# Kernel optimization log

Measured on AMD Instinct MI355X. Metric: run time of the kernel, lower is better.

The kernel has to match this reference:

```python
import jax, jax.numpy as jnp
import numpy as np

N_NODES = 10000

def rgcn_layer(x, edge_index, basis, comp, root, bias):
    # x: [N, Fin]; edge_index: [R, 2, E] int; basis: [B, Fin, Fout]; comp: [R, B]
    R, _, E = edge_index.shape
    N = x.shape[0]
    src = edge_index[:, 0]  # [R, E]
    dst = edge_index[:, 1]  # [R, E]
    # basis-decomposed per-relation weights: W_r = sum_b comp[r,b] * basis[b]
    W = jnp.einsum('rb,bio->rio', comp, basis)          # [R, Fin, Fout]
    x_src = x[src]                                       # [R, E, Fin] gather
    msg = jnp.einsum('rei,rio->reo', x_src, W)           # [R, E, Fout]
    # per-relation mean aggregation onto destination nodes
    seg = (jnp.arange(R, dtype=dst.dtype)[:, None] * N + dst).reshape(-1)  # [R*E]
    agg = jax.ops.segment_sum(msg.reshape(R * E, -1), seg, num_segments=R * N)
    deg = jax.ops.segment_sum(jnp.ones((R * E,), x.dtype), seg, num_segments=R * N)
    agg = agg / jnp.maximum(deg, 1.0)[:, None]
    agg = agg.reshape(R, N, -1).sum(0)                   # sum over relations
    return agg + x @ root + bias


def setup_inputs() -> dict:
    key = jax.random.key(0)
    ks = jax.random.split(key, 10)
    s = 0.05  # scale params for numerical sanity
    return {
        'x_drug': jax.random.normal(ks[0], (N_NODES, 2048), jnp.float32),
        'drug_w': jax.random.normal(ks[1], (2048, 128), jnp.float32) * s,
        'edge_index': jax.random.randint(ks[2], (100, 2, 5000), 0, N_NODES, jnp.int32),
        'basis1': jax.random.normal(ks[3], (8, 128, 64), jnp.float32) * s,
        'comp1': jax.random.normal(ks[4], (100, 8), jnp.float32) * s,
        'root1': jax.random.normal(ks[5], (128, 64), jnp.float32) * s,
        'bias1': jnp.zeros((64,), jnp.float32),
        'basis2': jax.random.normal(ks[6], (8, 64, 20), jnp.float32) * s,
        'comp2': jax.random.normal(ks[7], (100, 8), jnp.float32) * s,
        'root2': jax.random.normal(ks[8], (64, 20), jnp.float32) * s,
        'bias2': jnp.zeros((20,), jnp.float32),
    }


def reference(x_drug, drug_w, edge_index, basis1, comp1, root1, bias1,
              basis2, comp2, root2, bias2):
    x = x_drug @ drug_w                                   # dense projection [N, 128]
    h = rgcn_layer(x, edge_index, basis1, comp1, root1, bias1)   # [N, 64]
    h = jax.nn.relu(h)
    out = rgcn_layer(h, edge_index, basis2, comp2, root2, bias2)  # [N, 20]
    return out
```

## Files before the change

kernel.cpp:

```cpp
#include <hip/hip_runtime.h>

#define NN 10000
#define RR 100
#define EE 5000
#define D0 2048
#define D1 128
#define D2 64
#define D3 20
#define NE (RR*EE)
#define MAXD 128

using short8  = __attribute__((ext_vector_type(8))) short;
using float4e = __attribute__((ext_vector_type(4))) float;

typedef const __attribute__((address_space(1))) void g_void;
typedef __attribute__((address_space(3))) void l_void;

__device__ __forceinline__ unsigned short f2bf(float f) {
  unsigned int u = __float_as_uint(f);
  unsigned int r = u + 0x7fffu + ((u >> 16) & 1u);
  return (unsigned short)(r >> 16);
}
__device__ __forceinline__ float bf2f(unsigned short u) {
  return __uint_as_float(((unsigned int)u) << 16);
}
__device__ __forceinline__ unsigned int pk2(float lo, float hi) {
  return ((unsigned int)f2bf(hi) << 16) | (unsigned int)f2bf(lo);
}

#define CURB 10
#define WTBLK 1024
#define W1BLK 288
#define W2BLK 72
__global__ __launch_bounds__(256) void prep_kernel(
    const float* __restrict__ W, const float* __restrict__ root1,
    const float* __restrict__ basis1, const float* __restrict__ root2,
    const float* __restrict__ basis2, int4* __restrict__ cur4,
    unsigned short* __restrict__ Btw, unsigned short* __restrict__ Wc1T,
    unsigned short* __restrict__ Wc2T) {
  const int b = blockIdx.x, tid = threadIdx.x;
  if (b < CURB) {
    int i = b * 256 + tid;
    if (i < 2504) cur4[i] = make_int4(0, 0, 0, 0);
  } else if (b < CURB + WTBLK) {
    int idx = (b - CURB) * 256 + tid;
    int n = idx >> 11, k = idx & 2047;
    Btw[idx] = f2bf(W[(size_t)k * 128 + n]);
  } else if (b < CURB + WTBLK + W1BLK) {
    int idx = (b - CURB - WTBLK) * 256 + tid;
    int o = idx / 1152, j = idx - o * 1152;
    float v = (j < 128) ? root1[j * 64 + o] : basis1[(j - 128) * 64 + o];
    Wc1T[idx] = f2bf(v);
  } else {
    int idx = (b - CURB - WTBLK - W1BLK) * 256 + tid;
    int c = idx / 576, j = idx - c * 576;
    float v = 0.f;
    if (c < 20) v = (j < 64) ? root2[j * 20 + c] : basis2[(j - 64) * 20 + c];
    Wc2T[idx] = f2bf(v);
  }
}

__global__ void scatter_kernel(const int* __restrict__ ei,
                               int* __restrict__ cur, int* __restrict__ rec) {
  int gid = blockIdx.x * 256 + threadIdx.x;
  if (gid >= NE) return;
  int r = gid / EE, e = gid - r * EE;
  int s = ei[r * 2 * EE + e];
  int d = ei[r * 2 * EE + EE + e];
  int p = atomicAdd(&cur[d], 1);
  if (p < MAXD) rec[d * MAXD + p] = (r << 14) | s;
}

__global__ __launch_bounds__(256, 3) void gemm0_mfma(
    const float* __restrict__ A, const unsigned short* __restrict__ Btw,
    unsigned short* __restrict__ xb) {
  __shared__ __align__(16) unsigned short Asb[2][16 * 64];
  __shared__ __align__(16) unsigned short Bsb[3][128 * 64];
  const int tid = threadIdx.x;
  const int m0 = blockIdx.x * 16;
  const int wv = tid >> 6, lane = tid & 63;
  const int lrow = lane & 15, quad = lane >> 4;

  const int ar = tid >> 4, ag = tid & 15;
  const float* Ap = &A[(size_t)(m0 + ar) * D0 + ag * 4];
  const int aw = (ar * 128 + ((ag * 8) ^ ((ar & 7) << 4))) >> 1;

  const int rowB = wv * 32 + (lane >> 3);
  const int gch  = (lane & 7) ^ (lane >> 3);
  const unsigned short* BgBase = &Btw[(size_t)rowB * D0 + gch * 8];
  const int ldsB = wv * 2048;

  float4 a0, a1;

#define G0_LOADB(buf, c)                                                     \
  { _Pragma("unroll")                                                        \
    for (int i = 0; i < 4; i++) {                                            \
      __builtin_amdgcn_global_load_lds(                                      \
          (g_void*)(BgBase + (size_t)i * 8 * D0 + (c) * 64),                 \
          (l_void*)&Bsb[buf][ldsB + i * 512], 16, 0, 0);                     \
    } }

#define G0_LOADA(reg, c)  { reg = *(const float4*)(Ap + (c) * 64); }

#define G0_PACKA(reg, buf)                                              \
  { uint2 p0;                                                           \
    p0.x = pk2(reg.x, reg.y); p0.y = pk2(reg.z, reg.w);                 \
    *(uint2*)&Asb[buf][aw] = p0; }

#define G0_COMPUTE(abuf, bbuf)                                          \
  { const int aswz = (lrow & 7) << 4;                                   \
    _Pragma("unroll")                                                   \
    for (int kk = 0; kk < 2; kk++) {                                    \
      short8 af = *(const short8*)&Asb[abuf][(lrow * 128 + ((quad * 16 + kk * 64) ^ aswz)) >> 1]; \
      _Pragma("unroll")                                                 \
      for (int nt = 0; nt < 2; nt++) {                                  \
        const int brow = wv * 32 + nt * 16 + lrow;                      \
        short8 bfr = *(const short8*)&Bsb[bbuf][(brow * 128 + ((quad * 16 + kk * 64) ^ ((brow & 7) << 4))) >> 1]; \
        acc[nt] = __builtin_amdgcn_mfma_f32_16x16x32_bf16(af, bfr, acc[nt], 0, 0, 0); \
      }                                                                 \
    } }

  float4e acc[2];
#pragma unroll
  for (int i = 0; i < 2; i++) { acc[i][0]=0.f; acc[i][1]=0.f; acc[i][2]=0.f; acc[i][3]=0.f; }

  G0_LOADA(a0, 0);
  G0_LOADB(0, 0);
  G0_LOADB(1, 1);
  G0_PACKA(a0, 0);
  G0_LOADA(a1, 1);
  asm volatile("s_waitcnt vmcnt(5) lgkmcnt(0)\ns_barrier" ::: "memory");

#pragma unroll
  for (int c = 0; c < 32; c++) {
    if (c <= 29) {
      G0_LOADB((c + 2) % 3, c + 2);
      if ((c & 1) == 0) { G0_LOADA(a0, c + 2); }
      else              { G0_LOADA(a1, c + 2); }
      __builtin_amdgcn_sched_barrier(0);
    }
    G0_COMPUTE(c & 1, c % 3);
    if (c <= 30) {
      if (((c + 1) & 1) == 0) { G0_PACKA(a0, 0); }
      else                    { G0_PACKA(a1, 1); }
      asm volatile("s_waitcnt vmcnt(5) lgkmcnt(0)\ns_barrier" ::: "memory");
    }
  }

#pragma unroll
  for (int nt = 0; nt < 2; nt++) {
    const int col = wv * 32 + nt * 16 + lrow;
#pragma unroll
    for (int r = 0; r < 4; r++) {
      const int row = m0 + quad * 4 + r;
      xb[(size_t)row * D1 + col] = f2bf(acc[nt][r]);
    }
  }
}

__global__ __launch_bounds__(256) void agg1e_kernel(
    const unsigned short* __restrict__ xb, const int* __restrict__ cur,
    const int* __restrict__ rec, const float* __restrict__ comp,
    unsigned short* __restrict__ A1b) {
  __shared__ float s_comp[RR * 8];
  __shared__ float s_rcp[4][RR];
  const int tid = threadIdx.x;
  for (int i = tid; i < RR * 8; i += 256) s_comp[i] = comp[i];
  const int wv = tid >> 6, lane = tid & 63;
  const int n = blockIdx.x * 4 + wv;
  int* hist = (int*)&s_rcp[wv][0];
  for (int i = lane; i < RR; i += 64) hist[i] = 0;
  __syncthreads();
  int cnt = cur[n]; if (cnt > MAXD) cnt = MAXD;
  if (lane < cnt)      atomicAdd(&hist[rec[n * MAXD + lane] >> 14], 1);
  if (lane + 64 < cnt) atomicAdd(&hist[rec[n * MAXD + lane + 64] >> 14], 1);
  __syncthreads();
  for (int i = lane; i < RR; i += 64) {
    int h = hist[i];
    s_rcp[wv][i] = 1.0f / (float)h;
  }
  __syncthreads();

  float acc[8][2];
#pragma unroll
  for (int b = 0; b < 8; b++) { acc[b][0] = 0.f; acc[b][1] = 0.f; }
  const int beg = n * MAXD, end = beg + cnt;
  int idx = beg;
  for (; idx + 3 < end; idx += 4) {
    int rc[4]; float sc[4]; unsigned int xv[4];
#pragma unroll
    for (int u = 0; u < 4; u++) rc[u] = rec[idx + u];
#pragma unroll
    for (int u = 0; u < 4; u++) sc[u] = s_rcp[wv][rc[u] >> 14];
#pragma unroll
    for (int u = 0; u < 4; u++)
      xv[u] = *(const unsigned int*)&xb[(size_t)(rc[u] & 16383) * D1 + lane * 2];
#pragma unroll
    for (int u = 0; u < 4; u++) {
      const float* cb = &s_comp[(rc[u] >> 14) * 8];
      float x0 = __uint_as_float((xv[u] & 0xffffu) << 16);
      float x1 = __uint_as_float(xv[u] & 0xffff0000u);
#pragma unroll
      for (int b = 0; b < 8; b++) {
        float w = sc[u] * cb[b];
        acc[b][0] += w * x0;
        acc[b][1] += w * x1;
      }
    }
  }
  for (; idx < end; idx++) {
    int rc = rec[idx];
    float sc = s_rcp[wv][rc >> 14];
    unsigned int xv = *(const unsigned int*)&xb[(size_t)(rc & 16383) * D1 + lane * 2];
    const float* cb = &s_comp[(rc >> 14) * 8];
    float x0 = __uint_as_float((xv & 0xffffu) << 16);
    float x1 = __uint_as_float(xv & 0xffff0000u);
#pragma unroll
    for (int b = 0; b < 8; b++) {
      float w = sc * cb[b];
      acc[b][0] += w * x0;
      acc[b][1] += w * x1;
    }
  }
#pragma unroll
  for (int b = 0; b < 8; b++) {
    ushort2 o; o.x = f2bf(acc[b][0]); o.y = f2bf(acc[b][1]);
    *(ushort2*)&A1b[(size_t)n * 1024 + b * 128 + lane * 2] = o;
  }
}

__global__ __launch_bounds__(256) void agg2e_kernel(
    const unsigned short* __restrict__ hb, const int* __restrict__ cur,
    const int* __restrict__ rec, const float* __restrict__ comp,
    unsigned short* __restrict__ A2b) {
  __shared__ float s_comp[RR * 8];
  __shared__ float s_rcp[4][RR];
  const int tid = threadIdx.x;
  for (int i = tid; i < RR * 8; i += 256) s_comp[i] = comp[i];
  const int wv = tid >> 6, lane = tid & 63;
  const int n = blockIdx.x * 4 + wv;
  int* hist = (int*)&s_rcp[wv][0];
  for (int i = lane; i < RR; i += 64) hist[i] = 0;
  __syncthreads();
  int cnt = cur[n]; if (cnt > MAXD) cnt = MAXD;
  if (lane < cnt)      atomicAdd(&hist[rec[n * MAXD + lane] >> 14], 1);
  if (lane + 64 < cnt) atomicAdd(&hist[rec[n * MAXD + lane + 64] >> 14], 1);
  __syncthreads();
  for (int i = lane; i < RR; i += 64) {
    int h = hist[i];
    s_rcp[wv][i] = 1.0f / (float)h;
  }
  __syncthreads();

  float acc[8];
#pragma unroll
  for (int b = 0; b < 8; b++) acc[b] = 0.f;
  const int beg = n * MAXD, end = beg + cnt;
  int idx = beg;
  for (; idx + 3 < end; idx += 4) {
    int rc[4]; float sc[4]; float hv[4];
#pragma unroll
    for (int u = 0; u < 4; u++) rc[u] = rec[idx + u];
#pragma unroll
    for (int u = 0; u < 4; u++) sc[u] = s_rcp[wv][rc[u] >> 14];
#pragma unroll
    for (int u = 0; u < 4; u++)
      hv[u] = bf2f(hb[(size_t)(rc[u] & 16383) * D2 + lane]);
#pragma unroll
    for (int u = 0; u < 4; u++) {
      const float* cb = &s_comp[(rc[u] >> 14) * 8];
#pragma unroll
      for (int b = 0; b < 8; b++) acc[b] += sc[u] * cb[b] * hv[u];
    }
  }
  for (; idx < end; idx++) {
    int rc = rec[idx];
    float sc = s_rcp[wv][rc >> 14];
    float hv = bf2f(hb[(size_t)(rc & 16383) * D2 + lane]);
    const float* cb = &s_comp[(rc >> 14) * 8];
#pragma unroll
    for (int b = 0; b < 8; b++) acc[b] += sc * cb[b] * hv;
  }
#pragma unroll
  for (int b = 0; b < 8; b++)
    A2b[(size_t)n * 512 + b * 64 + lane] = f2bf(acc[b]);
}

__global__ __launch_bounds__(256) void hlayer_mfma(
    const unsigned short* __restrict__ xb, const unsigned short* __restrict__ A1b,
    const unsigned short* __restrict__ Wt, const float* __restrict__ bias1,
    unsigned short* __restrict__ hb) {
  __shared__ __align__(16) unsigned short Asb[2][32 * 64];
  __shared__ __align__(16) unsigned short Bsb[2][64 * 64];
  const int tid = threadIdx.x;
  const int m0 = blockIdx.x * 32;
  const int wv = tid >> 6, lane = tid & 63;
  const int lrow = lane & 15, quad = lane >> 4;
  const int mt = wv >> 1, nb = wv & 1;

  const int ar = tid >> 3, ac = tid & 7;
  int gr = m0 + ar; if (gr >= NN) gr = NN - 1;
  const unsigned short* Ax = &xb[(size_t)gr * D1 + ac * 8];
  const unsigned short* Aa = &A1b[(size_t)gr * 1024 + ac * 8];
  const int asw = (ar & 7) << 4;
  const int aw = (ar * 128 + ((ac * 16) ^ asw)) >> 1;

  const int br = tid >> 2, bq = tid & 3;
  const unsigned short* Bp = &Wt[(size_t)br * 1152 + bq * 16];
  const int bsw = (br & 7) << 4;
  const int bw0 = (br * 128 + ((bq * 32) ^ bsw)) >> 1;
  const int bw1 = (br * 128 + ((bq * 32 + 16) ^ bsw)) >> 1;

  uint4 ra, rb0, rb1;

#define H_LOADG(c)                                                       \
  { int kb = (c) * 64;                                                   \
    ra  = (kb < 128) ? *(const uint4*)(Ax + kb)                          \
                     : *(const uint4*)(Aa + (kb - 128));                 \
    rb0 = *(const uint4*)(Bp + kb);                                      \
    rb1 = *(const uint4*)(Bp + kb + 8); }

#define H_STOREL(buf)                                                    \
  { *(uint4*)&Asb[buf][aw]  = ra;                                        \
    *(uint4*)&Bsb[buf][bw0] = rb0;                                       \
    *(uint4*)&Bsb[buf][bw1] = rb1; }

#define H_COMPUTE(buf)                                                   \
  { const int arow = mt * 16 + lrow;                                     \
    const int aswz = (arow & 7) << 4;                                    \
    _Pragma("unroll")                                                    \
    for (int kk = 0; kk < 2; kk++) {                                     \
      short8 af = *(const short8*)&Asb[buf][(arow * 128 + ((quad * 16 + kk * 64) ^ aswz)) >> 1]; \
      _Pragma("unroll")                                                  \
      for (int nt = 0; nt < 2; nt++) {                                   \
        const int brow = nb * 32 + nt * 16 + lrow;                       \
        short8 bfr = *(const short8*)&Bsb[buf][(brow * 128 + ((quad * 16 + kk * 64) ^ ((brow & 7) << 4))) >> 1]; \
        acc[nt] = __builtin_amdgcn_mfma_f32_16x16x32_bf16(af, bfr, acc[nt], 0, 0, 0); \
      }                                                                  \
    } }

  float4e acc[2];
#pragma unroll
  for (int i = 0; i < 2; i++) { acc[i][0]=0.f; acc[i][1]=0.f; acc[i][2]=0.f; acc[i][3]=0.f; }

  H_LOADG(0);
  H_STOREL(0);
  __syncthreads();

#pragma unroll
  for (int c = 0; c < 18; c++) {
    if (c < 17) {
      H_LOADG(c + 1);
      __builtin_amdgcn_sched_barrier(0);
    }
    H_COMPUTE(c & 1);
    if (c < 17) H_STOREL((c + 1) & 1);
    __syncthreads();
  }

#pragma unroll
  for (int nt = 0; nt < 2; nt++) {
    int col = nb * 32 + nt * 16 + lrow;
    float bv = bias1[col];
#pragma unroll
    for (int r = 0; r < 4; r++) {
      int row = m0 + mt * 16 + quad * 4 + r;
      if (row < NN)
        hb[(size_t)row * D2 + col] = f2bf(fmaxf(acc[nt][r] + bv, 0.f));
    }
  }
}

__global__ __launch_bounds__(256) void out_mfma(
    const unsigned short* __restrict__ hb, const unsigned short* __restrict__ A2b,
    const unsigned short* __restrict__ Wt, const float* __restrict__ bias2,
    float* __restrict__ out) {
  __shared__ __align__(16) unsigned short Asb[2][32 * 64];
  __shared__ __align__(16) unsigned short Bsb[2][32 * 64];
  const int tid = threadIdx.x;
  const int m0 = blockIdx.x * 32;
  const int wv = tid >> 6, lane = tid & 63;
  const int lrow = lane & 15, quad = lane >> 4;
  const int mt = wv >> 1, ntn = wv & 1;

  const int ar = tid >> 3, ac = tid & 7;
  int gr = m0 + ar; if (gr >= NN) gr = NN - 1;
  const unsigned short* Ah = &hb[(size_t)gr * D2 + ac * 8];
  const unsigned short* Aa = &A2b[(size_t)gr * 512 + ac * 8];
  const unsigned short* Bp = &Wt[(size_t)ar * 576 + ac * 8];
  const int asw = (ar & 7) << 4;
  const int aw = (ar * 128 + ((ac * 16) ^ asw)) >> 1;

  uint4 ra, rb;

#define O_LOADG(c)                                                       \
  { int kb = (c) * 64;                                                   \
    ra = (kb < 64) ? *(const uint4*)(Ah)                                 \
                   : *(const uint4*)(Aa + (kb - 64));                    \
    rb = *(const uint4*)(Bp + kb); }

#define O_STOREL(buf)                                                    \
  { *(uint4*)&Asb[buf][aw] = ra;                                         \
    *(uint4*)&Bsb[buf][aw] = rb; }

#define O_COMPUTE(buf)                                                   \
  { const int arow = mt * 16 + lrow;                                     \
    const int aswz = (arow & 7) << 4;                                    \
    const int brow = ntn * 16 + lrow;                                    \
    const int bswz = (brow & 7) << 4;                                    \
    _Pragma("unroll")                                                    \
    for (int kk = 0; kk < 2; kk++) {                                     \
      short8 af = *(const short8*)&Asb[buf][(arow * 128 + ((quad * 16 + kk * 64) ^ aswz)) >> 1]; \
      short8 bfr = *(const short8*)&Bsb[buf][(brow * 128 + ((quad * 16 + kk * 64) ^ bswz)) >> 1]; \
      acc = __builtin_amdgcn_mfma_f32_16x16x32_bf16(af, bfr, acc, 0, 0, 0); \
    } }

  float4e acc;
  acc[0]=0.f; acc[1]=0.f; acc[2]=0.f; acc[3]=0.f;

  O_LOADG(0);
  O_STOREL(0);
  __syncthreads();

#pragma unroll
  for (int c = 0; c < 9; c++) {
    if (c < 8) {
      O_LOADG(c + 1);
      __builtin_amdgcn_sched_barrier(0);
    }
    O_COMPUTE(c & 1);
    if (c < 8) O_STOREL((c + 1) & 1);
    __syncthreads();
  }

  int col = ntn * 16 + lrow;
  if (col < D3) {
    float bv = bias2[col];
#pragma unroll
    for (int r = 0; r < 4; r++) {
      int row = m0 + mt * 16 + quad * 4 + r;
      if (row < NN)
        out[(size_t)row * D3 + col] = acc[r] + bv;
    }
  }
}

extern "C" void kernel_launch(void* const* d_in, const int* in_sizes, int n_in,
                              void* d_out, int out_size, void* d_ws,
                              size_t ws_size, hipStream_t stream) {
  const float* x_drug = (const float*)d_in[0];
  const float* drug_w = (const float*)d_in[1];
  const int*   ei     = (const int*)d_in[2];
  const float* basis1 = (const float*)d_in[3];
  const float* comp1  = (const float*)d_in[4];
  const float* root1  = (const float*)d_in[5];
  const float* bias1  = (const float*)d_in[6];
  const float* basis2 = (const float*)d_in[7];
  const float* comp2  = (const float*)d_in[8];
  const float* root2  = (const float*)d_in[9];
  const float* bias2  = (const float*)d_in[10];
  float* out = (float*)d_out;

  float* ws = (float*)d_ws;
  int*   cur  = (int*)ws;
  int*   rec  = cur + 10016;
  unsigned short* xb   = (unsigned short*)(rec + NN * MAXD);
  unsigned short* hb   = (unsigned short*)((float*)xb + 640000);
  unsigned short* Btw  = (unsigned short*)((float*)hb + 320000);
  unsigned short* Wc1T = (unsigned short*)((float*)Btw + 131072);
  unsigned short* Wc2T = (unsigned short*)((float*)Wc1T + 36864);
  float* R1 = (float*)Wc2T + 9216;
  unsigned short* A1b = (unsigned short*)R1;
  unsigned short* A2b = (unsigned short*)R1;

  prep_kernel<<<CURB + WTBLK + W1BLK + W2BLK, 256, 0, stream>>>(
      drug_w, root1, basis1, root2, basis2, (int4*)cur, Btw, Wc1T, Wc2T);

  scatter_kernel<<<(NE + 255) / 256, 256, 0, stream>>>(ei, cur, rec);

  gemm0_mfma<<<NN / 16, 256, 0, stream>>>(x_drug, Btw, xb);

  agg1e_kernel<<<NN / 4, 256, 0, stream>>>(xb, cur, rec, comp1, A1b);
  hlayer_mfma<<<(NN + 31) / 32, 256, 0, stream>>>(xb, A1b, Wc1T, bias1, hb);

  agg2e_kernel<<<NN / 4, 256, 0, stream>>>(hb, cur, rec, comp2, A2b);
  out_mfma<<<(NN + 31) / 32, 256, 0, stream>>>(hb, A2b, Wc2T, bias2, out);
}
```

Baseline: 147.6 us.

## Retile dense projection GEMM into 64x32 tiles with half-K B staging

The first dense GEMM now gives each block 64 rows by 32 output columns, with each wave owning 16 private rows, instead of giving each block 16 rows by all 128 columns. The 32-column B slice is staged into LDS in two large halves, which removes the per-K-step block barriers, and A loads use a deeper three-register prefetch. This cuts how much of B each block reads. In exchange, each A row is now read by four blocks, so more fp32 A traffic goes through cache, and LDS use rises while the occupancy hint drops from three blocks to two.

After: 183.0 us. 1.24x slower.

```diff
diff --git a/kernel.cpp b/kernel.cpp
--- a/kernel.cpp
+++ b/kernel.cpp
@@ -71,89 +71,105 @@
   if (p < MAXD) rec[d * MAXD + p] = (r << 14) | s;
 }
 
-__global__ __launch_bounds__(256, 3) void gemm0_mfma(
+__global__ __launch_bounds__(256, 2) void gemm0_mfma(
     const float* __restrict__ A, const unsigned short* __restrict__ Btw,
     unsigned short* __restrict__ xb) {
-  __shared__ __align__(16) unsigned short Asb[2][16 * 64];
-  __shared__ __align__(16) unsigned short Bsb[3][128 * 64];
+  __shared__ __align__(16) unsigned short Bsb[32 * 1024];
+  __shared__ __align__(16) unsigned short Asb[4][2][16 * 64];
   const int tid = threadIdx.x;
-  const int m0 = blockIdx.x * 16;
   const int wv = tid >> 6, lane = tid & 63;
+  const int mtile = blockIdx.x >> 2, nt4 = blockIdx.x & 3;
+  const int m0 = mtile * 64;
+  const int n0 = nt4 * 32;
   const int lrow = lane & 15, quad = lane >> 4;
 
-  const int ar = tid >> 4, ag = tid & 15;
-  const float* Ap = &A[(size_t)(m0 + ar) * D0 + ag * 4];
-  const int aw = (ar * 128 + ((ag * 8) ^ ((ar & 7) << 4))) >> 1;
-
-  const int rowB = wv * 32 + (lane >> 3);
-  const int gch  = (lane & 7) ^ (lane >> 3);
-  const unsigned short* BgBase = &Btw[(size_t)rowB * D0 + gch * 8];
-  const int ldsB = wv * 2048;
-
-  float4 a0, a1;
-
-#define G0_LOADB(buf, c)                                                     \
-  { _Pragma("unroll")                                                        \
-    for (int i = 0; i < 4; i++) {                                            \
-      __builtin_amdgcn_global_load_lds(                                      \
-          (g_void*)(BgBase + (size_t)i * 8 * D0 + (c) * 64),                 \
-          (l_void*)&Bsb[buf][ldsB + i * 512], 16, 0, 0);                     \
+  const int ar = lane >> 2, aq = lane & 3;
+  int gra = m0 + wv * 16 + ar; if (gra >= NN) gra = NN - 1;
+  const float* Ap = &A[(size_t)gra * D0 + aq * 16];
+  const int asw = (ar & 7) << 4;
+  const int aw0 = (ar * 128 + ((aq * 32) ^ asw)) >> 1;
+  const int aw1 = (ar * 128 + ((aq * 32 + 16) ^ asw)) >> 1;
+
+#define G0_STAGEB(half)                                                     \
+  { _Pragma("unroll")                                                       \
+    for (int j = 0; j < 16; j++) {                                          \
+      const int it  = wv * 16 + j;                                          \
+      const int row = it >> 1;                                              \
+      const int kb  = (it & 1) * 512;                                       \
+      const unsigned short* src = &Btw[(size_t)(n0 + row) * D0 +            \
+          (half) * 1024 + kb + ((lane * 8) ^ ((row & 7) << 3))];            \
+      __builtin_amdgcn_global_load_lds((g_void*)src,                        \
+          (l_void*)&Bsb[it * 512 + lane * 8], 16, 0, 0);                    \
     } }
 
-#define G0_LOADA(reg, c)  { reg = *(const float4*)(Ap + (c) * 64); }
-
-#define G0_PACKA(reg, buf)                                              \
-  { uint2 p0;                                                           \
-    p0.x = pk2(reg.x, reg.y); p0.y = pk2(reg.z, reg.w);                 \
-    *(uint2*)&Asb[buf][aw] = p0; }
-
-#define G0_COMPUTE(abuf, bbuf)                                          \
-  { const int aswz = (lrow & 7) << 4;                                   \
-    _Pragma("unroll")                                                   \
-    for (int kk = 0; kk < 2; kk++) {                                    \
-      short8 af = *(const short8*)&Asb[abuf][(lrow * 128 + ((quad * 16 + kk * 64) ^ aswz)) >> 1]; \
-      _Pragma("unroll")                                                 \
-      for (int nt = 0; nt < 2; nt++) {                                  \
-        const int brow = wv * 32 + nt * 16 + lrow;                      \
-        short8 bfr = *(const short8*)&Bsb[bbuf][(brow * 128 + ((quad * 16 + kk * 64) ^ ((brow & 7) << 4))) >> 1]; \
-        acc[nt] = __builtin_amdgcn_mfma_f32_16x16x32_bf16(af, bfr, acc[nt], 0, 0, 0); \
-      }                                                                 \
+#define G0_LOADA(R, c)                                                      \
+  { _Pragma("unroll")                                                       \
+    for (int j = 0; j < 4; j++)                                             \
+      R[j] = *(const float4*)(Ap + (size_t)(c) * 64 + j * 4); }
+
+#define G0_PACKA(R, buf)                                                    \
+  { uint4 p, q;                                                             \
+    p.x = pk2(R[0].x, R[0].y); p.y = pk2(R[0].z, R[0].w);                   \
+    p.z = pk2(R[1].x, R[1].y); p.w = pk2(R[1].z, R[1].w);                   \
+    q.x = pk2(R[2].x, R[2].y); q.y = pk2(R[2].z, R[2].w);                   \
+    q.z = pk2(R[3].x, R[3].y); q.w = pk2(R[3].z, R[3].w);                   \
+    *(uint4*)&Asb[wv][buf][aw0] = p;                                        \
+    *(uint4*)&Asb[wv][buf][aw1] = q; }
+
+#define G0_COMPUTE(abuf, c)                                                 \
+  { const int aswz = (lrow & 7) << 4;                                       \
+    _Pragma("unroll")                                                       \
+    for (int kk = 0; kk < 2; kk++) {                                        \
+      short8 af = *(const short8*)&Asb[wv][abuf][(lrow * 128 + ((kk * 64 + quad * 16) ^ aswz)) >> 1]; \
+      _Pragma("unroll")                                                     \
+      for (int ntl = 0; ntl < 2; ntl++) {                                   \
+        const int brow = ntl * 16 + lrow;                                   \
+        short8 bfr = *(const short8*)&Bsb[brow * 1024 + ((((c & 15) * 128 + kk * 64 + quad * 16) ^ ((brow & 7) << 4)) >> 1)]; \
+        acc[ntl] = __builtin_amdgcn_mfma_f32_16x16x32_bf16(af, bfr, acc[ntl], 0, 0, 0); \
+      }                                                                     \
     } }
 
+  float4 Ra[4], Rb[4], Rc[4];
   float4e acc[2];
 #pragma unroll
   for (int i = 0; i < 2; i++) { acc[i][0]=0.f; acc[i][1]=0.f; acc[i][2]=0.f; acc[i][3]=0.f; }
 
-  G0_LOADA(a0, 0);
-  G0_LOADB(0, 0);
-  G0_LOADB(1, 1);
-  G0_PACKA(a0, 0);
-  G0_LOADA(a1, 1);
-  asm volatile("s_waitcnt vmcnt(5) lgkmcnt(0)\ns_barrier" ::: "memory");
+  G0_STAGEB(0);
+  G0_LOADA(Ra, 0);
+  G0_LOADA(Rb, 1);
+  G0_LOADA(Rc, 2);
+  G0_PACKA(Ra, 0);
+  __syncthreads();
 
 #pragma unroll
   for (int c = 0; c < 32; c++) {
-    if (c <= 29) {
-      G0_LOADB((c + 2) % 3, c + 2);
-      if ((c & 1) == 0) { G0_LOADA(a0, c + 2); }
-      else              { G0_LOADA(a1, c + 2); }
+    if (c == 16) {
+      __syncthreads();
+      G0_STAGEB(1);
+      __syncthreads();
+    }
+    if (c < 29) {
+      if (c % 3 == 0)      { G0_LOADA(Ra, c + 3); }
+      else if (c % 3 == 1) { G0_LOADA(Rb, c + 3); }
+      else                 { G0_LOADA(Rc, c + 3); }
       __builtin_amdgcn_sched_barrier(0);
     }
-    G0_COMPUTE(c & 1, c % 3);
-    if (c <= 30) {
-      if (((c + 1) & 1) == 0) { G0_PACKA(a0, 0); }
-      else                    { G0_PACKA(a1, 1); }
-      asm volatile("s_waitcnt vmcnt(5) lgkmcnt(0)\ns_barrier" ::: "memory");
-    }
-  }
-
-#pragma unroll
-  for (int nt = 0; nt < 2; nt++) {
-    const int col = wv * 32 + nt * 16 + lrow;
+    G0_COMPUTE(c & 1, c);
+    if (c < 31) {
+      if ((c + 1) % 3 == 0)      { G0_PACKA(Ra, (c + 1) & 1); }
+      else if ((c + 1) % 3 == 1) { G0_PACKA(Rb, (c + 1) & 1); }
+      else                       { G0_PACKA(Rc, (c + 1) & 1); }
+    }
+  }
+
+#pragma unroll
+  for (int ntl = 0; ntl < 2; ntl++) {
+    const int col = n0 + ntl * 16 + lrow;
 #pragma unroll
     for (int r = 0; r < 4; r++) {
-      const int row = m0 + quad * 4 + r;
-      xb[(size_t)row * D1 + col] = f2bf(acc[nt][r]);
+      const int row = m0 + wv * 16 + quad * 4 + r;
+      if (row < NN)
+        xb[(size_t)row * D1 + col] = f2bf(acc[ntl][r]);
     }
   }
 }
@@ -478,7 +494,7 @@
 
   scatter_kernel<<<(NE + 255) / 256, 256, 0, stream>>>(ei, cur, rec);
 
-  gemm0_mfma<<<NN / 16, 256, 0, stream>>>(x_drug, Btw, xb);
+  gemm0_mfma<<<157 * 4, 256, 0, stream>>>(x_drug, Btw, xb);
 
   agg1e_kernel<<<NN / 4, 256, 0, stream>>>(xb, cur, rec, comp1, A1b);
   hlayer_mfma<<<(NN + 31) / 32, 256, 0, stream>>>(xb, A1b, Wc1T, bias1, hb);
```
